# Optimization experiments

Measured on AMD Instinct MI355X. Metric: run time of the kernel, lower is better.

Reference implementation:

```python
import jax, jax.numpy as jnp
import numpy as np

N = 4096
IN_F = 256
OUT_F = 128
H = 2
ALPHA = 0.2  # leaky relu slope
NEG_INF = -9e15  # matches -9000000000000000.0 in the torch code


def setup_inputs() -> dict:
    key = jax.random.key(0)
    k_x, k_adj, k_w, k_a = jax.random.split(key, 4)
    x = jax.random.normal(k_x, (N, IN_F), dtype=jnp.float32)
    adj = (jax.random.uniform(k_adj, (N, N)) < 0.005).astype(jnp.float32)
    # xavier_uniform with gain=1.414 as in the torch module
    gain = 1.414
    bound_w = gain * np.sqrt(6.0 / (IN_F + OUT_F))
    W = jax.random.uniform(k_w, (H, IN_F, OUT_F), minval=-bound_w, maxval=bound_w, dtype=jnp.float32)
    bound_a = gain * np.sqrt(6.0 / (2 * OUT_F + 1))
    a = jax.random.uniform(k_a, (H, 2 * OUT_F, 1), minval=-bound_a, maxval=bound_a, dtype=jnp.float32)
    return {"x": x, "adj": adj, "W": W, "a": a}


def reference(x, adj, W, a):
    # Dense multi-head GAT layer (eval mode: dropout is identity).
    n = x.shape[0]
    h, _, f_out = W.shape
    adj = adj + jnp.eye(n, dtype=adj.dtype)  # add self loops
    xt = jnp.einsum('nf,hfo->hno', x, W)  # [H, N, F_out]
    # The repeat_interleave/repeat + concat + matmul(a) in the original is
    # exactly the additive decomposition: score[h,i,j] = xt[h,i]@a1[h] + xt[h,j]@a2[h]
    a1 = a[:, :f_out, 0]   # [H, F_out] (applied to target/query node i)
    a2 = a[:, f_out:, 0]   # [H, F_out] (applied to source node j)
    e1 = jnp.einsum('hno,ho->hn', xt, a1)  # [H, N]
    e2 = jnp.einsum('hno,ho->hn', xt, a2)  # [H, N]
    scores = jax.nn.leaky_relu(e1[:, :, None] + e2[:, None, :], negative_slope=ALPHA)  # [H,N,N]
    scores = jnp.where(adj > 0, scores, jnp.asarray(NEG_INF, scores.dtype))
    attn = jax.nn.softmax(scores, axis=-1)
    h_prime = jnp.einsum('hij,hjo->hio', attn, xt)  # [H, N, F_out]
    # concat=True branch: torch .view(N, H*F_out) on contiguous [H,N,F] -> same as reshape
    return jax.nn.elu(h_prime.reshape(n, h * f_out))
```

## Files before the change

kernel.cpp:

```cpp
#include <hip/hip_runtime.h>
#include <math.h>

#define IN_F 256
#define OUT_F 128
#define NHEAD 2
#define ALPHA 0.2f
#define NN 4096
#define NCAP 128

typedef __attribute__((ext_vector_type(8))) short short8;
typedef __attribute__((ext_vector_type(4))) float f32x4;
typedef const __attribute__((address_space(1))) void* gas_ptr;
typedef __attribute__((address_space(3))) void* las_ptr;

__device__ __forceinline__ void async_copy16(const void* g, void* l) {
  __builtin_amdgcn_global_load_lds((gas_ptr)g, (las_ptr)l, 16, 0, 0);
}

__device__ __forceinline__ ushort f2bf(float f) {
  unsigned u = __float_as_uint(f);
  u += 0x7fffu + ((u >> 16) & 1u);
  return (ushort)(u >> 16);
}

__device__ __forceinline__ float lrelu(float t) { return t > 0.f ? t : ALPHA * t; }

__global__ __launch_bounds__(256) void prep_w(
    const float* __restrict__ W, ushort* __restrict__ Wt) {
  int p = blockIdx.x * 256 + threadIdx.x;
  int h = p >> 13;
  int rem = p & 8191;
  int c = rem >> 7;
  int o = rem & 127;
  const float* wsrc = W + h * (IN_F * OUT_F) + (4 * c) * OUT_F + o;
  ushort4 ov;
  ov.x = f2bf(wsrc[0 * OUT_F]);
  ov.y = f2bf(wsrc[1 * OUT_F]);
  ov.z = f2bf(wsrc[2 * OUT_F]);
  ov.w = f2bf(wsrc[3 * OUT_F]);
  *(ushort4*)(Wt + ((size_t)h * OUT_F + o) * IN_F + 4 * c) = ov;
}

__global__ __launch_bounds__(256) void gemm_mfma(
    const float* __restrict__ x, const ushort* __restrict__ Wt,
    const float* __restrict__ a,
    float* __restrict__ xt, float* __restrict__ e1, float* __restrict__ e2) {
  __shared__ ushort sA[32 * 64];
  __shared__ ushort sB[128 * 64];
  __shared__ float sa[2 * OUT_F];
  __shared__ float se1[32], se2[32];

  const int h = blockIdx.y;
  const int rowBase = blockIdx.x * 32;
  const int tid = threadIdx.x;
  const int wave = tid >> 6, lane = tid & 63;
  const int wr = wave & 1, wc = wave >> 1;
  const int q = lane >> 4, l16 = lane & 15;
  const int ar = tid >> 3;
  const int ak = (tid & 7) * 8;

  const float* xrow = x + (size_t)(rowBase + ar) * IN_F + ak;
  float4 ax[8];
#pragma unroll
  for (int c = 0; c < 4; ++c) {
    ax[2 * c]     = *(const float4*)(xrow + 64 * c);
    ax[2 * c + 1] = *(const float4*)(xrow + 64 * c + 4);
  }

  sa[tid] = a[h * (2 * OUT_F) + tid];

  f32x4 acc[4];
#pragma unroll
  for (int i = 0; i < 4; ++i) acc[i] = (f32x4)(0.0f);

  const char* wbase = (const char*)(Wt + (size_t)h * (OUT_F * IN_F));

#pragma unroll
  for (int c = 0; c < 4; ++c) {
    const int k0 = c * 64;
#pragma unroll
    for (int it = 0; it < 4; ++it) {
      int g = it * 256 + tid;
      int r = g >> 3, c8 = g & 7;
      async_copy16(wbase + r * 512 + k0 * 2 + c8 * 16,
                   (char*)sB + (size_t)(it * 256 + wave * 64) * 16);
    }
    {
      float4 va = ax[2 * c], vb = ax[2 * c + 1];
      union { short8 s8; ushort u[8]; } pk;
      pk.u[0] = f2bf(va.x); pk.u[1] = f2bf(va.y);
      pk.u[2] = f2bf(va.z); pk.u[3] = f2bf(va.w);
      pk.u[4] = f2bf(vb.x); pk.u[5] = f2bf(vb.y);
      pk.u[6] = f2bf(vb.z); pk.u[7] = f2bf(vb.w);
      *(short8*)(sA + ar * 64 + ak) = pk.s8;
    }
    __syncthreads();

#pragma unroll
    for (int ks = 0; ks < 64; ks += 32) {
      short8 af = *(const short8*)(sA + (wr * 16 + l16) * 64 + ks + q * 8);
#pragma unroll
      for (int ct = 0; ct < 4; ++ct) {
        int col = wc * 64 + ct * 16 + l16;
        short8 bf = *(const short8*)(sB + col * 64 + ks + q * 8);
        acc[ct] = __builtin_amdgcn_mfma_f32_16x16x32_bf16(af, bf, acc[ct], 0, 0, 0);
      }
    }
    __syncthreads();
  }

#pragma unroll
  for (int ct = 0; ct < 4; ++ct) {
    int col = wc * 64 + ct * 16 + l16;
#pragma unroll
    for (int reg = 0; reg < 4; ++reg) {
      int row = rowBase + wr * 16 + q * 4 + reg;
      xt[((size_t)h * NN + row) * OUT_F + col] = acc[ct][reg];
    }
  }

  float pe1[4], pe2[4];
#pragma unroll
  for (int reg = 0; reg < 4; ++reg) { pe1[reg] = 0.f; pe2[reg] = 0.f; }
#pragma unroll
  for (int ct = 0; ct < 4; ++ct) {
    int col = wc * 64 + ct * 16 + l16;
    float a1v = sa[col], a2v = sa[OUT_F + col];
#pragma unroll
    for (int reg = 0; reg < 4; ++reg) {
      pe1[reg] = fmaf(acc[ct][reg], a1v, pe1[reg]);
      pe2[reg] = fmaf(acc[ct][reg], a2v, pe2[reg]);
    }
  }
#pragma unroll
  for (int off = 1; off < 16; off <<= 1) {
#pragma unroll
    for (int reg = 0; reg < 4; ++reg) {
      pe1[reg] += __shfl_xor(pe1[reg], off, 64);
      pe2[reg] += __shfl_xor(pe2[reg], off, 64);
    }
  }
  if (wc == 0 && l16 == 0) {
#pragma unroll
    for (int reg = 0; reg < 4; ++reg) {
      int r = wr * 16 + q * 4 + reg;
      se1[r] = pe1[reg];
      se2[r] = pe2[reg];
    }
  }
  __syncthreads();
  if (wc == 1 && l16 == 0) {
#pragma unroll
    for (int reg = 0; reg < 4; ++reg) {
      int r = wr * 16 + q * 4 + reg;
      se1[r] += pe1[reg];
      se2[r] += pe2[reg];
    }
  }
  __syncthreads();
  if (tid < 32) {
    e1[(size_t)h * NN + rowBase + tid] = se1[tid];
    e2[(size_t)h * NN + rowBase + tid] = se2[tid];
  }
}

__global__ __launch_bounds__(256) void gat_aggregate(
    const float* __restrict__ adj, const float* __restrict__ xt,
    const float* __restrict__ e1, const float* __restrict__ e2,
    float* __restrict__ out) {
  __shared__ int s_nbr[4][NCAP];
  __shared__ float s_p0[4][NCAP];
  __shared__ float s_p1[4][NCAP];

  const int wave = threadIdx.x >> 6;
  const int lane = threadIdx.x & 63;
  const int i = blockIdx.x * 4 + wave;

  const float4* row4 = (const float4*)(adj + (size_t)i * NN);
  float4 v[16];
#pragma unroll
  for (int c = 0; c < 16; ++c) v[c] = row4[lane + c * 64];

  const unsigned long long lt = (1ull << lane) - 1ull;
  int cnt = 0;
#pragma unroll
  for (int c = 0; c < 16; ++c) {
    float vals[4] = {v[c].x, v[c].y, v[c].z, v[c].w};
#pragma unroll
    for (int s = 0; s < 4; ++s) {
      int j = (c * 64 + lane) * 4 + s;
      bool hit = (vals[s] > 0.f) || (j == i);
      unsigned long long mask = __ballot(hit);
      if (hit) {
        int pos = cnt + (int)__popcll(mask & lt);
        if (pos < NCAP) s_nbr[wave][pos] = j;
      }
      cnt += (int)__popcll(mask);
    }
  }
  const int m = cnt < NCAP ? cnt : NCAP;

  const float e10 = e1[i];
  const float e11 = e1[NN + i];
  float t0[2], t1[2];
  float mx0 = -3.0e38f, mx1 = -3.0e38f;
#pragma unroll
  for (int r = 0; r < 2; ++r) {
    int k = lane + r * 64;
    if (k < m) {
      int j = s_nbr[wave][k];
      t0[r] = lrelu(e10 + e2[j]);
      t1[r] = lrelu(e11 + e2[NN + j]);
      mx0 = fmaxf(mx0, t0[r]);
      mx1 = fmaxf(mx1, t1[r]);
    } else {
      t0[r] = -3.0e38f;
      t1[r] = -3.0e38f;
    }
  }
#pragma unroll
  for (int off = 32; off > 0; off >>= 1) {
    mx0 = fmaxf(mx0, __shfl_xor(mx0, off, 64));
    mx1 = fmaxf(mx1, __shfl_xor(mx1, off, 64));
  }

  float s0 = 0.f, s1 = 0.f;
#pragma unroll
  for (int r = 0; r < 2; ++r) {
    int k = lane + r * 64;
    if (k < m) {
      float p0 = __expf(t0[r] - mx0);
      float p1 = __expf(t1[r] - mx1);
      s_p0[wave][k] = p0;
      s_p1[wave][k] = p1;
      s0 += p0;
      s1 += p1;
    }
  }
#pragma unroll
  for (int off = 32; off > 0; off >>= 1) {
    s0 += __shfl_xor(s0, off, 64);
    s1 += __shfl_xor(s1, off, 64);
  }

  const int h = lane >> 5;
  const int o4 = (lane & 31) * 4;
  const float linv = 1.0f / (h ? s1 : s0);
  const float* pw = h ? s_p1[wave] : s_p0[wave];
  const int* nb = s_nbr[wave];
  const float* xth = xt + (size_t)h * NN * OUT_F + o4;

  f32x4 acc = (f32x4)(0.0f);
  int k = 0;
  for (; k + 4 <= m; k += 4) {
    int j0 = nb[k], j1 = nb[k + 1], j2 = nb[k + 2], j3 = nb[k + 3];
    float w0 = pw[k], w1 = pw[k + 1], w2 = pw[k + 2], w3 = pw[k + 3];
    f32x4 x0 = *(const f32x4*)(xth + (size_t)j0 * OUT_F);
    f32x4 x1 = *(const f32x4*)(xth + (size_t)j1 * OUT_F);
    f32x4 x2 = *(const f32x4*)(xth + (size_t)j2 * OUT_F);
    f32x4 x3 = *(const f32x4*)(xth + (size_t)j3 * OUT_F);
    acc += w0 * x0;
    acc += w1 * x1;
    acc += w2 * x2;
    acc += w3 * x3;
  }
  for (; k < m; ++k) {
    f32x4 xv = *(const f32x4*)(xth + (size_t)nb[k] * OUT_F);
    acc += pw[k] * xv;
  }

  f32x4 r;
#pragma unroll
  for (int e = 0; e < 4; ++e) {
    float av = acc[e] * linv;
    r[e] = av > 0.f ? av : (__expf(av) - 1.0f);
  }
  *(f32x4*)(out + ((size_t)h * NN + i) * OUT_F + o4) = r;
}

extern "C" void kernel_launch(void* const* d_in, const int* in_sizes, int n_in,
                              void* d_out, int out_size, void* d_ws, size_t ws_size,
                              hipStream_t stream) {
  const float* x   = (const float*)d_in[0];
  const float* adj = (const float*)d_in[1];
  const float* W   = (const float*)d_in[2];
  const float* a   = (const float*)d_in[3];
  float* out = (float*)d_out;

  float* xt = (float*)d_ws;
  float* e1 = xt + (size_t)NHEAD * NN * OUT_F;
  float* e2 = e1 + (size_t)NHEAD * NN;
  ushort* Wt = (ushort*)(e2 + (size_t)NHEAD * NN);

  prep_w<<<64, 256, 0, stream>>>(W, Wt);
  gemm_mfma<<<dim3(NN / 32, NHEAD), 256, 0, stream>>>(x, Wt, a, xt, e1, e2);
  gat_aggregate<<<NN / 4, 256, 0, stream>>>(adj, xt, e1, e2, out);
}
```

Measured before the change: 112.5 us.

## Move adjacency scan into GEMM launch to overlap with projection

The adjacency row scan that builds neighbor lists moves out of the aggregation kernel and into extra blocks of the GEMM launch. It now writes compact neighbor indices and counts to global workspace. The bandwidth-heavy dense adj read (64 MB) can then run concurrently with the MFMA projection. The aggregation kernel only reads the small neighbor lists, at the cost of extra workspace and a global write/read round trip.

```diff
diff --git a/kernel.cpp b/kernel.cpp
--- a/kernel.cpp
+++ b/kernel.cpp
@@ -41,19 +41,50 @@
   *(ushort4*)(Wt + ((size_t)h * OUT_F + o) * IN_F + 4 * c) = ov;
 }
 
-__global__ __launch_bounds__(256) void gemm_mfma(
+__global__ __launch_bounds__(256) void gemm_scan(
     const float* __restrict__ x, const ushort* __restrict__ Wt,
-    const float* __restrict__ a,
-    float* __restrict__ xt, float* __restrict__ e1, float* __restrict__ e2) {
+    const float* __restrict__ a, const float* __restrict__ adj,
+    float* __restrict__ xt, float* __restrict__ e1, float* __restrict__ e2,
+    int* __restrict__ g_nbr, int* __restrict__ g_cnt) {
   __shared__ ushort sA[32 * 64];
   __shared__ ushort sB[128 * 64];
   __shared__ float sa[2 * OUT_F];
   __shared__ float se1[32], se2[32];
 
-  const int h = blockIdx.y;
-  const int rowBase = blockIdx.x * 32;
   const int tid = threadIdx.x;
   const int wave = tid >> 6, lane = tid & 63;
+
+  if (blockIdx.x >= 256) {
+    const int i = (blockIdx.x - 256) * 4 + wave;
+    const float4* row4 = (const float4*)(adj + (size_t)i * NN);
+    float4 v[16];
+#pragma unroll
+    for (int c = 0; c < 16; ++c) v[c] = row4[lane + c * 64];
+
+    const unsigned long long lt = (1ull << lane) - 1ull;
+    int* nrow = g_nbr + (size_t)i * NCAP;
+    int cnt = 0;
+#pragma unroll
+    for (int c = 0; c < 16; ++c) {
+      float vals[4] = {v[c].x, v[c].y, v[c].z, v[c].w};
+#pragma unroll
+      for (int s = 0; s < 4; ++s) {
+        int j = (c * 64 + lane) * 4 + s;
+        bool hit = (vals[s] > 0.f) || (j == i);
+        unsigned long long mask = __ballot(hit);
+        if (hit) {
+          int pos = cnt + (int)__popcll(mask & lt);
+          if (pos < NCAP) nrow[pos] = j;
+        }
+        cnt += (int)__popcll(mask);
+      }
+    }
+    if (lane == 0) g_cnt[i] = cnt < NCAP ? cnt : NCAP;
+    return;
+  }
+
+  const int h = blockIdx.x >> 7;
+  const int rowBase = (blockIdx.x & 127) * 32;
   const int wr = wave & 1, wc = wave >> 1;
   const int q = lane >> 4, l16 = lane & 15;
   const int ar = tid >> 3;
@@ -164,8 +195,9 @@
   }
 }
 
-__global__ __launch_bounds__(256) void gat_aggregate(
-    const float* __restrict__ adj, const float* __restrict__ xt,
+__global__ __launch_bounds__(256) void gat2(
+    const int* __restrict__ g_nbr, const int* __restrict__ g_cnt,
+    const float* __restrict__ xt,
     const float* __restrict__ e1, const float* __restrict__ e2,
     float* __restrict__ out) {
   __shared__ int s_nbr[4][NCAP];
@@ -176,29 +208,18 @@
   const int lane = threadIdx.x & 63;
   const int i = blockIdx.x * 4 + wave;
 
-  const float4* row4 = (const float4*)(adj + (size_t)i * NN);
-  float4 v[16];
-#pragma unroll
-  for (int c = 0; c < 16; ++c) v[c] = row4[lane + c * 64];
-
-  const unsigned long long lt = (1ull << lane) - 1ull;
-  int cnt = 0;
-#pragma unroll
-  for (int c = 0; c < 16; ++c) {
-    float vals[4] = {v[c].x, v[c].y, v[c].z, v[c].w};
-#pragma unroll
-    for (int s = 0; s < 4; ++s) {
-      int j = (c * 64 + lane) * 4 + s;
-      bool hit = (vals[s] > 0.f) || (j == i);
-      unsigned long long mask = __ballot(hit);
-      if (hit) {
-        int pos = cnt + (int)__popcll(mask & lt);
-        if (pos < NCAP) s_nbr[wave][pos] = j;
-      }
-      cnt += (int)__popcll(mask);
-    }
-  }
-  const int m = cnt < NCAP ? cnt : NCAP;
+  const int m = g_cnt[i];
+  const int* nrow = g_nbr + (size_t)i * NCAP;
+
+  int jj[2] = {-1, -1};
+#pragma unroll
+  for (int r = 0; r < 2; ++r) {
+    int k = lane + r * 64;
+    if (k < m) {
+      jj[r] = nrow[k];
+      s_nbr[wave][k] = jj[r];
+    }
+  }
 
   const float e10 = e1[i];
   const float e11 = e1[NN + i];
@@ -208,7 +229,7 @@
   for (int r = 0; r < 2; ++r) {
     int k = lane + r * 64;
     if (k < m) {
-      int j = s_nbr[wave][k];
+      int j = jj[r];
       t0[r] = lrelu(e10 + e2[j]);
       t1[r] = lrelu(e11 + e2[NN + j]);
       mx0 = fmaxf(mx0, t0[r]);
@@ -291,8 +312,10 @@
   float* e1 = xt + (size_t)NHEAD * NN * OUT_F;
   float* e2 = e1 + (size_t)NHEAD * NN;
   ushort* Wt = (ushort*)(e2 + (size_t)NHEAD * NN);
+  int* g_nbr = (int*)(Wt + (size_t)NHEAD * OUT_F * IN_F);
+  int* g_cnt = g_nbr + (size_t)NN * NCAP;
 
   prep_w<<<64, 256, 0, stream>>>(W, Wt);
-  gemm_mfma<<<dim3(NN / 32, NHEAD), 256, 0, stream>>>(x, Wt, a, xt, e1, e2);
-  gat_aggregate<<<NN / 4, 256, 0, stream>>>(adj, xt, e1, e2, out);
-}
+  gemm_scan<<<256 + NN / 4, 256, 0, stream>>>(x, Wt, a, adj, xt, e1, e2, g_nbr, g_cnt);
+  gat2<<<NN / 4, 256, 0, stream>>>(g_nbr, g_cnt, xt, e1, e2, out);
+}
```

Result: no change. 112.9 us (+0.4%).
